# Performance work log

Measured on AMD Instinct MI355X. Metric: run time of the kernel, lower is better.

The kernel has to match this reference:

```python
import jax, jax.numpy as jnp
import numpy as np

ALPHA = 0.2  # LeakyReLU negative slope


def _gat_layer(x, edge_src, edge_dst, edge_embed, a, a2, concat):
    # torch: edge_h = cat(input[edge[0]], input[edge[1]], edge_embed).t(); scatter rows = edge[0]
    h = jnp.concatenate([x[edge_src], x[edge_dst], edge_embed], axis=1)  # [E, 2F+R]
    edge_m = h @ a.T                                                      # [E, D]
    powers = -jax.nn.leaky_relu(edge_m @ a2, ALPHA)                       # [E]
    edge_e = jnp.exp(powers)                                              # [E]
    N = x.shape[0]
    rowsum = jax.ops.segment_sum(edge_e, edge_src, num_segments=N)        # [N]
    rowsum = jnp.where(rowsum == 0.0, 1e-12, rowsum)
    h_prime = jax.ops.segment_sum(edge_e[:, None] * edge_m, edge_src, num_segments=N)  # [N, D]
    h_prime = h_prime / rowsum[:, None]
    return jax.nn.elu(h_prime) if concat else h_prime


def _spgat_forward(entity_embeddings, relation_embed, edge_embed, a, a2, W,
                   a_out, a2_out, edge_list, edge_type, edge_list_nhop, edge_type_nhop):
    nheads = a.shape[0]
    # concatenate 1-hop and n-hop edges (as in torch forward of the attention layer)
    src = jnp.concatenate([edge_list[0], edge_list_nhop[0]], axis=0)
    dst = jnp.concatenate([edge_list[1], edge_list_nhop[1]], axis=0)
    ee_nhop = relation_embed[edge_type_nhop[:, 0]] + relation_embed[edge_type_nhop[:, 1]]
    ee_all = jnp.concatenate([edge_embed, ee_nhop], axis=0)               # [E+E2, R]
    heads = [_gat_layer(entity_embeddings, src, dst, ee_all, a[i], a2[i], True)
             for i in range(nheads)]
    x = jnp.concatenate(heads, axis=1)                                    # [N, H*F] (dropout = identity, eval)
    out_relation_1 = relation_embed @ W                                   # [n_rel, H*F]
    ee2 = out_relation_1[edge_type]
    ee2_nhop = out_relation_1[edge_type_nhop[:, 0]] + out_relation_1[edge_type_nhop[:, 1]]
    ee2_all = jnp.concatenate([ee2, ee2_nhop], axis=0)                    # [E+E2, H*F]
    x = jax.nn.elu(_gat_layer(x, src, dst, ee2_all, a_out, a2_out, False))
    return x, out_relation_1


def setup_inputs() -> dict:
    key = jax.random.key(0)
    N, F, R, NREL, E, E2, H = 50000, 128, 128, 500, 150000, 30000, 2
    ks = jax.random.split(key, 12)

    def xavier(k, shape):
        fan_in, fan_out = shape[-1], shape[-2]
        std = 1.414 * np.sqrt(2.0 / (fan_in + fan_out))
        return (jax.random.normal(k, shape, dtype=jnp.float32) * std).astype(jnp.float32)

    return {
        "entity_embeddings": jax.random.normal(ks[0], (N, F), dtype=jnp.float32),
        "relation_embed": jax.random.normal(ks[1], (NREL, R), dtype=jnp.float32),
        "edge_embed": jax.random.normal(ks[2], (E, R), dtype=jnp.float32),
        "edge_list": jax.random.randint(ks[3], (2, E), 0, N),
        "edge_type": jax.random.randint(ks[4], (E,), 0, NREL),
        "edge_list_nhop": jax.random.randint(ks[5], (2, E2), 0, N),
        "edge_type_nhop": jax.random.randint(ks[6], (E2, 2), 0, NREL),
        "a": xavier(ks[7], (H, F, 2 * F + R)),            # per-head a: [D, 2F+R]
        "a2": xavier(ks[8], (H, 1, F))[:, 0, :],          # per-head a_2: [D]
        "W": xavier(ks[9], (R, H * F)),
        "a_out": xavier(ks[10], (H * F, 3 * H * F)),      # out layer: in=H*F, nrela=H*F
        "a2_out": xavier(ks[11], (1, H * F))[0],
    }


def reference(entity_embeddings, relation_embed, edge_embed, edge_list, edge_type,
              edge_list_nhop, edge_type_nhop, a, a2, W, a_out, a2_out):
    return _spgat_forward(entity_embeddings, relation_embed, edge_embed, a, a2, W,
                          a_out, a2_out, edge_list, edge_type, edge_list_nhop, edge_type_nhop)
```

## Files before the change

### kernel.cpp

```cpp
#include <hip/hip_runtime.h>
#include <cstdint>
#include <cstddef>

#define N_NODES 50000
#define MP1     50048
#define NRELC   500
#define E1      150000
#define MP2     150016
#define E2N     30000
#define ETOT    180000
#define ALPHA_F 0.2f
#define NBSCAN  49

typedef __attribute__((ext_vector_type(8))) short bf16x8;
typedef __attribute__((ext_vector_type(4))) float f32x4;

__device__ __forceinline__ float bf2f(unsigned short s) {
  return __uint_as_float((unsigned)s << 16);
}
__device__ __forceinline__ unsigned short f2bf(float f) {
  unsigned u = __float_as_uint(f);
  u += 0x7fff + ((u >> 16) & 1);
  return (unsigned short)(u >> 16);
}

__global__ void zero_int(int* __restrict__ p, int n) {
  int i = blockIdx.x * blockDim.x + threadIdx.x;
  if (i < n) p[i] = 0;
}

__global__ void build_count(const int* __restrict__ el, const int* __restrict__ elnh,
                            int* __restrict__ src, int* __restrict__ dst,
                            int* __restrict__ cnt) {
  int e = blockIdx.x * blockDim.x + threadIdx.x;
  if (e >= ETOT) return;
  int s, d;
  if (e < E1) { s = el[e];  d = el[E1 + e]; }
  else        { int k = e - E1; s = elnh[k]; d = elnh[E2N + k]; }
  src[e] = s; dst[e] = d;
  atomicAdd(&cnt[s], 1);
}

__global__ __launch_bounds__(256) void block_scan(const int* __restrict__ cnt,
                                                  int* __restrict__ rowptr,
                                                  int* __restrict__ blocksum) {
  __shared__ int wsum[4];
  const int tid  = threadIdx.x;
  const int lane = tid & 63;
  const int wave = tid >> 6;
  const int idx  = blockIdx.x * 1024 + tid * 4;
  int v0 = 0, v1 = 0, v2 = 0, v3 = 0;
  if (idx + 3 < N_NODES) {
    int4 t = *reinterpret_cast<const int4*>(cnt + idx);
    v0 = t.x; v1 = t.y; v2 = t.z; v3 = t.w;
  } else {
    if (idx + 0 < N_NODES) v0 = cnt[idx + 0];
    if (idx + 1 < N_NODES) v1 = cnt[idx + 1];
    if (idx + 2 < N_NODES) v2 = cnt[idx + 2];
  }
  const int tsum = v0 + v1 + v2 + v3;
  int incl = tsum;
#pragma unroll
  for (int off = 1; off < 64; off <<= 1) {
    int u = __shfl_up(incl, off);
    if (lane >= off) incl += u;
  }
  if (lane == 63) wsum[wave] = incl;
  __syncthreads();
  int woff = 0;
#pragma unroll
  for (int w = 0; w < 4; ++w)
    if (w < wave) woff += wsum[w];
  const int ebase = woff + incl - tsum;
  if (idx + 0 < N_NODES) rowptr[idx + 0] = ebase;
  if (idx + 1 < N_NODES) rowptr[idx + 1] = ebase + v0;
  if (idx + 2 < N_NODES) rowptr[idx + 2] = ebase + v0 + v1;
  if (idx + 3 < N_NODES) rowptr[idx + 3] = ebase + v0 + v1 + v2;
  if (tid == 255) blocksum[blockIdx.x] = woff + incl;
}

__global__ void scan_blocksums(int* __restrict__ blocksum, int* __restrict__ rowptr) {
  const int lane = threadIdx.x & 63;
  int v = (lane < NBSCAN) ? blocksum[lane] : 0;
  int incl = v;
#pragma unroll
  for (int off = 1; off < 64; off <<= 1) {
    int u = __shfl_up(incl, off);
    if (lane >= off) incl += u;
  }
  if (lane < NBSCAN) blocksum[lane] = incl - v;
  if (lane == 63) rowptr[N_NODES] = incl;
}

__global__ void add_offsets(int* __restrict__ rowptr, const int* __restrict__ blocksum,
                            int* __restrict__ pos) {
  int i = blockIdx.x * 256 + threadIdx.x;
  if (i < N_NODES) {
    int r = rowptr[i] + blocksum[i >> 10];
    rowptr[i] = r;
    pos[i] = r;
  }
}

__global__ void fill_csr(const int* __restrict__ src, int* __restrict__ pos, int* __restrict__ csr) {
  int e = blockIdx.x * blockDim.x + threadIdx.x;
  if (e >= ETOT) return;
  int p = atomicAdd(&pos[src[e]], 1);
  csr[p] = e;
}

#define PK_TOT (32768 + 32768 + 65536 + 65536 + 32768 + 131072)
__global__ void pack_all(const float* __restrict__ a, const float* __restrict__ W,
                         const float* __restrict__ ao,
                         float* __restrict__ weea3f, float* __restrict__ wtw,
                         float* __restrict__ wa3o,
                         unsigned short* __restrict__ wxa_bf,
                         unsigned short* __restrict__ weea3_bf,
                         unsigned short* __restrict__ wx1a_bf) {
  int i = blockIdx.x * blockDim.x + threadIdx.x;
  if (i >= PK_TOT) return;
  if (i < 32768) {
    int c = i >> 7, k = i & 127;
    int h = c >> 7, d = c & 127;
    weea3f[i] = a[h * 49152 + d * 384 + 256 + k];
  } else if (i < 65536) {
    int j = i - 32768;
    int n = j >> 7, k = j & 127;
    wtw[j] = W[k * 256 + n];
  } else if (i < 131072) {
    int j = i - 65536;
    int d = j >> 8, k = j & 255;
    wa3o[j] = ao[d * 768 + 512 + k];
  } else if (i < 196608) {
    int j = i - 131072;
    int c = j >> 7, k = j & 127;
    int h = c >> 8, part = (c >> 7) & 1, d = c & 127;
    wxa_bf[j] = f2bf(a[h * 49152 + d * 384 + part * 128 + k]);
  } else if (i < 229376) {
    int j = i - 196608;
    int c = j >> 7, k = j & 127;
    int h = c >> 7, d = c & 127;
    weea3_bf[j] = f2bf(a[h * 49152 + d * 384 + 256 + k]);
  } else {
    int j = i - 229376;
    int c = j >> 8, k = j & 255;
    int part = c >> 8, d = c & 255;
    wx1a_bf[j] = f2bf(ao[d * 768 + part * 256 + k]);
  }
}

__global__ __launch_bounds__(256) void gemm_bt_f32(
    const float* __restrict__ A, const float* __restrict__ Wt,
    float* __restrict__ C, int M, int N, int K) {
  __shared__ float As[32][132];
  __shared__ float Bs[32][132];
  const int bm = blockIdx.x * 128;
  const int bn = blockIdx.y * 128;
  const int tid = threadIdx.x;
  const int tx = tid & 15;
  const int ty = tid >> 4;
  float acc[8][8];
#pragma unroll
  for (int i = 0; i < 8; ++i)
#pragma unroll
    for (int j = 0; j < 8; ++j) acc[i][j] = 0.f;

  const int lr = tid >> 3;
  const int lc = (tid & 7) << 2;

  for (int k0 = 0; k0 < K; k0 += 32) {
#pragma unroll
    for (int i = 0; i < 4; ++i) {
      const int row = lr + (i << 5);
      float4 av = make_float4(0.f, 0.f, 0.f, 0.f);
      float4 bv = make_float4(0.f, 0.f, 0.f, 0.f);
      const int ga = bm + row, gb = bn + row;
      if (ga < M) av = *reinterpret_cast<const float4*>(A + (size_t)ga * K + k0 + lc);
      if (gb < N) bv = *reinterpret_cast<const float4*>(Wt + (size_t)gb * K + k0 + lc);
      As[lc + 0][row] = av.x; As[lc + 1][row] = av.y; As[lc + 2][row] = av.z; As[lc + 3][row] = av.w;
      Bs[lc + 0][row] = bv.x; Bs[lc + 1][row] = bv.y; Bs[lc + 2][row] = bv.z; Bs[lc + 3][row] = bv.w;
    }
    __syncthreads();
    for (int kk = 0; kk < 32; ++kk) {
      float a8[8], b8[8];
      *(float4*)&a8[0] = *(const float4*)&As[kk][ty * 8];
      *(float4*)&a8[4] = *(const float4*)&As[kk][ty * 8 + 4];
      *(float4*)&b8[0] = *(const float4*)&Bs[kk][tx * 8];
      *(float4*)&b8[4] = *(const float4*)&Bs[kk][tx * 8 + 4];
#pragma unroll
      for (int i = 0; i < 8; ++i)
#pragma unroll
        for (int j = 0; j < 8; ++j) acc[i][j] = fmaf(a8[i], b8[j], acc[i][j]);
    }
    __syncthreads();
  }
#pragma unroll
  for (int i = 0; i < 8; ++i) {
    const int gr = bm + ty * 8 + i;
    if (gr < M) {
      float4 v0 = make_float4(acc[i][0], acc[i][1], acc[i][2], acc[i][3]);
      float4 v1 = make_float4(acc[i][4], acc[i][5], acc[i][6], acc[i][7]);
      *reinterpret_cast<float4*>(C + (size_t)gr * N + bn + tx * 8) = v0;
      *reinterpret_cast<float4*>(C + (size_t)gr * N + bn + tx * 8 + 4) = v1;
    }
  }
}

template <typename TA, int K>
__global__ __launch_bounds__(256) void gemm_mfma(
    const TA* __restrict__ A, const unsigned short* __restrict__ Wt,
    unsigned short* __restrict__ C, int Mreal, int N) {
  __shared__ __align__(16) unsigned short lds[2][8192];
  const int tid  = threadIdx.x;
  const int wave = tid >> 6;
  const int lane = tid & 63;
  const int bm = blockIdx.x * 128;
  const int bn = blockIdx.y * 128;
  const int wr = wave >> 1, wc = wave & 1;
  constexpr int NT = K / 32;

  f32x4 acc[4][4] = {};

  const int rb   = lane & 15;
  const int cofs = ((lane >> 4) ^ (lane & 3)) << 3;

  auto stageB = [&](int buf, int kt) {
#pragma unroll
    for (int j = 0; j < 2; ++j) {
      const int o   = (wave * 2 + j) * 1024 + lane * 16;
      const int row = o >> 6;
      const int sc  = (o & 63) ^ ((row & 3) << 4);
      const char* g = (const char*)Wt + (size_t)(bn + row) * (K * 2) + kt * 64 + sc;
      __builtin_amdgcn_global_load_lds(
          (const __attribute__((address_space(1))) void*)g,
          (__attribute__((address_space(3))) void*)&lds[buf][4096 + (wave * 2 + j) * 512],
          16, 0, 0);
    }
  };
  auto stageA = [&](int buf, int kt) {
    if constexpr (sizeof(TA) == 2) {
#pragma unroll
      for (int j = 0; j < 2; ++j) {
        const int o   = (wave * 2 + j) * 1024 + lane * 16;
        const int row = o >> 6;
        const int sc  = (o & 63) ^ ((row & 3) << 4);
        const char* g = (const char*)A + (size_t)(bm + row) * (K * 2) + kt * 64 + sc;
        __builtin_amdgcn_global_load_lds(
            (const __attribute__((address_space(1))) void*)g,
            (__attribute__((address_space(3))) void*)&lds[buf][(wave * 2 + j) * 512],
            16, 0, 0);
      }
    } else {
#pragma unroll
      for (int p = 0; p < 2; ++p) {
        const int o   = p * 4096 + tid * 16;
        const int row = o >> 6;
        const int ke  = ((o & 63) ^ ((row & 3) << 4)) >> 1;
        const int gr  = bm + row;
        float v[8];
#pragma unroll
        for (int q = 0; q < 8; ++q) v[q] = 0.f;
        if (gr < Mreal) {
          const float* gp = (const float*)A + (size_t)gr * K + kt * 32 + ke;
          float4 u0 = *(const float4*)gp;
          float4 u1 = *(const float4*)(gp + 4);
          v[0] = u0.x; v[1] = u0.y; v[2] = u0.z; v[3] = u0.w;
          v[4] = u1.x; v[5] = u1.y; v[6] = u1.z; v[7] = u1.w;
        }
        bf16x8 pk;
#pragma unroll
        for (int q = 0; q < 8; ++q) pk[q] = (short)f2bf(v[q]);
        *(bf16x8*)&lds[buf][o >> 1] = pk;
      }
    }
  };

  stageA(0, 0); stageB(0, 0);
  for (int t = 0; t < NT; ++t) {
    __syncthreads();
    if (t + 1 < NT) { stageA((t + 1) & 1, t + 1); stageB((t + 1) & 1, t + 1); }
    const int buf = t & 1;
    bf16x8 af[4], bfr[4];
#pragma unroll
    for (int m = 0; m < 4; ++m)
      af[m] = *(const bf16x8*)&lds[buf][(rb + 16 * m + 64 * wr) * 32 + cofs];
#pragma unroll
    for (int n = 0; n < 4; ++n)
      bfr[n] = *(const bf16x8*)&lds[buf][4096 + (rb + 16 * n + 64 * wc) * 32 + cofs];
#pragma unroll
    for (int m = 0; m < 4; ++m)
#pragma unroll
      for (int n = 0; n < 4; ++n)
        acc[m][n] = __builtin_amdgcn_mfma_f32_16x16x32_bf16(af[m], bfr[n], acc[m][n], 0, 0, 0);
  }

  const int ccol = bn + wc * 64 + rb;
  const int crow = bm + wr * 64 + ((lane >> 4) << 2);
#pragma unroll
  for (int m = 0; m < 4; ++m)
#pragma unroll
    for (int n = 0; n < 4; ++n)
#pragma unroll
      for (int r = 0; r < 4; ++r)
        C[(size_t)(crow + 16 * m + r) * N + ccol + 16 * n] = f2bf(acc[m][n][r]);
}

__global__ __launch_bounds__(256) void agg1(
    const unsigned short* __restrict__ xa, const unsigned short* __restrict__ eeA31,
    const float* __restrict__ relA3, const int* __restrict__ rowptr,
    const int* __restrict__ csr, const int* __restrict__ dst,
    const int* __restrict__ etnh, const float* __restrict__ a2,
    unsigned short* __restrict__ x1) {
  int w = blockIdx.x * 4 + (threadIdx.x >> 6);
  int n = w >> 1, h = w & 1;
  if (n >= N_NODES) return;
  int l = threadIdx.x & 63;
  float w2a = a2[h * 128 + l];
  float w2b = a2[h * 128 + 64 + l];
  const unsigned short* xan = xa + (size_t)n * 512 + h * 256;
  float s0 = bf2f(xan[l]), s1 = bf2f(xan[64 + l]);
  float acc0 = 0.f, acc1 = 0.f, rs = 0.f;
  int p0 = rowptr[n], p1 = rowptr[n + 1];
  for (int p = p0; p < p1; ++p) {
    int e = csr[p];
    int d = dst[e];
    const unsigned short* xad = xa + (size_t)d * 512 + h * 256 + 128;
    float m0 = s0 + bf2f(xad[l]);
    float m1 = s1 + bf2f(xad[64 + l]);
    if (e < E1) {
      const unsigned short* ee = eeA31 + (size_t)e * 256 + h * 128;
      m0 += bf2f(ee[l]); m1 += bf2f(ee[64 + l]);
    } else {
      int k = e - E1;
      int t0 = etnh[2 * k], t1 = etnh[2 * k + 1];
      const float* r0 = relA3 + t0 * 256 + h * 128;
      const float* r1 = relA3 + t1 * 256 + h * 128;
      m0 += r0[l] + r1[l];
      m1 += r0[64 + l] + r1[64 + l];
    }
    float dot = m0 * w2a + m1 * w2b;
#pragma unroll
    for (int off = 32; off; off >>= 1) dot += __shfl_xor(dot, off);
    float lk = dot > 0.f ? dot : ALPHA_F * dot;
    float ev = __expf(-lk);
    acc0 = fmaf(ev, m0, acc0);
    acc1 = fmaf(ev, m1, acc1);
    rs += ev;
  }
  if (rs == 0.f) rs = 1e-12f;
  float inv = 1.f / rs;
  float h0 = acc0 * inv, h1 = acc1 * inv;
  h0 = h0 > 0.f ? h0 : (__expf(h0) - 1.f);
  h1 = h1 > 0.f ? h1 : (__expf(h1) - 1.f);
  x1[(size_t)n * 256 + h * 128 + l] = f2bf(h0);
  x1[(size_t)n * 256 + h * 128 + 64 + l] = f2bf(h1);
}

__global__ __launch_bounds__(256) void agg2(
    const unsigned short* __restrict__ x1a, const float* __restrict__ rel2,
    const int* __restrict__ rowptr, const int* __restrict__ csr,
    const int* __restrict__ dst, const int* __restrict__ etype,
    const int* __restrict__ etnh, const float* __restrict__ a2o,
    float* __restrict__ out) {
  int n = blockIdx.x * 4 + (threadIdx.x >> 6);
  if (n >= N_NODES) return;
  int l = threadIdx.x & 63;
  float w2[4], s[4], acc[4] = {0.f, 0.f, 0.f, 0.f};
#pragma unroll
  for (int j = 0; j < 4; ++j) {
    w2[j] = a2o[j * 64 + l];
    s[j] = bf2f(x1a[(size_t)n * 512 + j * 64 + l]);
  }
  float rs = 0.f;
  int p0 = rowptr[n], p1 = rowptr[n + 1];
  for (int p = p0; p < p1; ++p) {
    int e = csr[p];
    int d = dst[e];
    const unsigned short* xd = x1a + (size_t)d * 512 + 256;
    float m[4];
    if (e < E1) {
      int t = etype[e];
      const float* r = rel2 + t * 256;
#pragma unroll
      for (int j = 0; j < 4; ++j) m[j] = s[j] + bf2f(xd[j * 64 + l]) + r[j * 64 + l];
    } else {
      int k = e - E1;
      int t0 = etnh[2 * k], t1 = etnh[2 * k + 1];
      const float* r0 = rel2 + t0 * 256;
      const float* r1 = rel2 + t1 * 256;
#pragma unroll
      for (int j = 0; j < 4; ++j) m[j] = s[j] + bf2f(xd[j * 64 + l]) + r0[j * 64 + l] + r1[j * 64 + l];
    }
    float dot = 0.f;
#pragma unroll
    for (int j = 0; j < 4; ++j) dot = fmaf(m[j], w2[j], dot);
#pragma unroll
    for (int off = 32; off; off >>= 1) dot += __shfl_xor(dot, off);
    float lk = dot > 0.f ? dot : ALPHA_F * dot;
    float ev = __expf(-lk);
#pragma unroll
    for (int j = 0; j < 4; ++j) acc[j] = fmaf(ev, m[j], acc[j]);
    rs += ev;
  }
  if (rs == 0.f) rs = 1e-12f;
  float inv = 1.f / rs;
#pragma unroll
  for (int j = 0; j < 4; ++j) {
    float hv = acc[j] * inv;
    hv = hv > 0.f ? hv : (__expf(hv) - 1.f);
    out[(size_t)n * 256 + j * 64 + l] = hv;
  }
}

extern "C" void kernel_launch(void* const* d_in, const int* in_sizes, int n_in,
                              void* d_out, int out_size, void* d_ws, size_t ws_size,
                              hipStream_t stream) {
  const float* x    = (const float*)d_in[0];
  const float* rel  = (const float*)d_in[1];
  const float* eemb = (const float*)d_in[2];
  const int*   el   = (const int*)d_in[3];
  const int*   et   = (const int*)d_in[4];
  const int*   elnh = (const int*)d_in[5];
  const int*   etnh = (const int*)d_in[6];
  const float* a    = (const float*)d_in[7];
  const float* a2   = (const float*)d_in[8];
  const float* W    = (const float*)d_in[9];
  const float* aout = (const float*)d_in[10];
  const float* a2o  = (const float*)d_in[11];

  char* ws = (char*)d_ws;
  size_t cur = 0;
  auto alloc = [&](size_t bytes) {
    size_t o = cur;
    cur = (cur + bytes + 511) & ~(size_t)511;
    return o;
  };
  int* src     = (int*)(ws + alloc((size_t)ETOT * 4));
  int* dstv    = (int*)(ws + alloc((size_t)ETOT * 4));
  int* rowptr  = (int*)(ws + alloc((size_t)(N_NODES + 1) * 4));
  int* pos     = (int*)(ws + alloc((size_t)N_NODES * 4));
  int* csr     = (int*)(ws + alloc((size_t)ETOT * 4));
  int* bsum    = (int*)(ws + alloc((size_t)64 * 4));
  float* weea3f = (float*)(ws + alloc((size_t)256 * 128 * 4));
  float* wtw    = (float*)(ws + alloc((size_t)256 * 128 * 4));
  float* wa3o   = (float*)(ws + alloc((size_t)256 * 256 * 4));
  unsigned short* wxa_bf   = (unsigned short*)(ws + alloc((size_t)512 * 128 * 2));
  unsigned short* weea3_bf = (unsigned short*)(ws + alloc((size_t)256 * 128 * 2));
  unsigned short* wx1a_bf  = (unsigned short*)(ws + alloc((size_t)512 * 256 * 2));
  float* relA3 = (float*)(ws + alloc((size_t)NRELC * 256 * 4));
  float* rel2  = (float*)(ws + alloc((size_t)NRELC * 256 * 4));
  unsigned short* x1B = (unsigned short*)(ws + alloc((size_t)MP1 * 256 * 2));
  unsigned short* xaB = (unsigned short*)(ws + alloc((size_t)MP1 * 512 * 2));
  unsigned short* eeB = (unsigned short*)(ws + alloc((size_t)MP2 * 256 * 2));
  (void)ws_size; (void)in_sizes; (void)n_in; (void)out_size;

  float* out_x    = (float*)d_out;
  float* out_rel1 = out_x + (size_t)N_NODES * 256;

  zero_int<<<(N_NODES + 255) / 256, 256, 0, stream>>>(pos, N_NODES);
  build_count<<<(ETOT + 255) / 256, 256, 0, stream>>>(el, elnh, src, dstv, pos);
  block_scan<<<NBSCAN, 256, 0, stream>>>(pos, rowptr, bsum);
  scan_blocksums<<<1, 64, 0, stream>>>(bsum, rowptr);
  add_offsets<<<(N_NODES + 255) / 256, 256, 0, stream>>>(rowptr, bsum, pos);
  fill_csr<<<(ETOT + 255) / 256, 256, 0, stream>>>(src, pos, csr);

  pack_all<<<(PK_TOT + 255) / 256, 256, 0, stream>>>(a, W, aout, weea3f, wtw, wa3o,
                                                     wxa_bf, weea3_bf, wx1a_bf);

  gemm_mfma<float, 128><<<dim3(MP1 / 128, 4), 256, 0, stream>>>(x, wxa_bf, xaB, N_NODES, 512);
  gemm_mfma<float, 128><<<dim3(MP2 / 128, 2), 256, 0, stream>>>(eemb, weea3_bf, eeB, E1, 256);
  gemm_bt_f32<<<dim3((NRELC + 127) / 128, 2), 256, 0, stream>>>(rel, weea3f, relA3, NRELC, 256, 128);

  agg1<<<(N_NODES * 2 + 3) / 4, 256, 0, stream>>>(xaB, eeB, relA3, rowptr, csr, dstv, etnh, a2, x1B);

  gemm_bt_f32<<<dim3((NRELC + 127) / 128, 2), 256, 0, stream>>>(rel, wtw, out_rel1, NRELC, 256, 128);
  gemm_bt_f32<<<dim3((NRELC + 127) / 128, 2), 256, 0, stream>>>(out_rel1, wa3o, rel2, NRELC, 256, 256);

  gemm_mfma<unsigned short, 256><<<dim3(MP1 / 128, 4), 256, 0, stream>>>(x1B, wx1a_bf, xaB, MP1, 512);

  agg2<<<(N_NODES + 3) / 4, 256, 0, stream>>>(xaB, rel2, rowptr, csr, dstv, et, etnh, a2o, out_x);
}
```

Measured before the change: 496.4 us.

## Precompute attention logits via folded a2·A vectors and batch edge gathers

```diff
diff --git a/kernel.cpp b/kernel.cpp
--- a/kernel.cpp
+++ b/kernel.cpp
@@ -11,6 +11,7 @@
 #define ETOT    180000
 #define ALPHA_F 0.2f
 #define NBSCAN  49
+#define NDBLK   ((N_NODES + 3) / 4)
 
 typedef __attribute__((ext_vector_type(8))) short bf16x8;
 typedef __attribute__((ext_vector_type(4))) float f32x4;
@@ -109,14 +110,18 @@
   csr[p] = e;
 }
 
-#define PK_TOT (32768 + 32768 + 65536 + 65536 + 32768 + 131072)
+#define PK_COPY (32768 + 32768 + 65536 + 65536 + 32768 + 131072)
+#define PK_TOT  (PK_COPY + 768 + 768)
 __global__ void pack_all(const float* __restrict__ a, const float* __restrict__ W,
-                         const float* __restrict__ ao,
+                         const float* __restrict__ ao, const float* __restrict__ a2,
+                         const float* __restrict__ a2o,
                          float* __restrict__ weea3f, float* __restrict__ wtw,
                          float* __restrict__ wa3o,
                          unsigned short* __restrict__ wxa_bf,
                          unsigned short* __restrict__ weea3_bf,
-                         unsigned short* __restrict__ wx1a_bf) {
+                         unsigned short* __restrict__ wx1a_bf,
+                         float* __restrict__ vaL1,
+                         float* __restrict__ vaL2) {
   int i = blockIdx.x * blockDim.x + threadIdx.x;
   if (i >= PK_TOT) return;
   if (i < 32768) {
@@ -141,11 +146,25 @@
     int c = j >> 7, k = j & 127;
     int h = c >> 7, d = c & 127;
     weea3_bf[j] = f2bf(a[h * 49152 + d * 384 + 256 + k]);
-  } else {
+  } else if (i < PK_COPY) {
     int j = i - 229376;
     int c = j >> 8, k = j & 255;
     int part = c >> 8, d = c & 255;
     wx1a_bf[j] = f2bf(ao[d * 768 + part * 256 + k]);
+  } else if (i < PK_COPY + 768) {
+    int j = i - PK_COPY;
+    int v = j >> 8, rem = j & 255, h = rem >> 7, k = rem & 127;
+    float s = 0.f;
+    for (int d = 0; d < 128; ++d)
+      s = fmaf(a2[h * 128 + d], a[h * 49152 + d * 384 + v * 128 + k], s);
+    vaL1[(v * 2 + h) * 128 + k] = s;
+  } else {
+    int j = i - PK_COPY - 768;
+    int v = j >> 8, k = j & 255;
+    float s = 0.f;
+    for (int d = 0; d < 256; ++d)
+      s = fmaf(a2o[d], ao[d * 768 + v * 256 + k], s);
+    vaL2[v * 256 + k] = s;
   }
 }
 
@@ -206,10 +225,12 @@
   }
 }
 
-template <typename TA, int K>
+template <typename TA, int K, int NS>
 __global__ __launch_bounds__(256) void gemm_mfma(
     const TA* __restrict__ A, const unsigned short* __restrict__ Wt,
-    unsigned short* __restrict__ C, int Mreal, int N) {
+    unsigned short* __restrict__ C,
+    const float* __restrict__ va, float* __restrict__ sout,
+    int Mreal, int N) {
   __shared__ __align__(16) unsigned short lds[2][8192];
   const int tid  = threadIdx.x;
   const int wave = tid >> 6;
@@ -220,6 +241,14 @@
   constexpr int NT = K / 32;
 
   f32x4 acc[4][4] = {};
+  float sacc[2][NS > 0 ? NS : 1];
+  if constexpr (NS > 0) {
+#pragma unroll
+    for (int p = 0; p < 2; ++p)
+#pragma unroll
+      for (int s = 0; s < NS; ++s) sacc[p][s] = 0.f;
+  }
+  const bool do_s = (NS > 0) && (blockIdx.y == 0);
 
   const int rb   = lane & 15;
   const int cofs = ((lane >> 4) ^ (lane & 3)) << 3;
@@ -267,6 +296,15 @@
           v[0] = u0.x; v[1] = u0.y; v[2] = u0.z; v[3] = u0.w;
           v[4] = u1.x; v[5] = u1.y; v[6] = u1.z; v[7] = u1.w;
         }
+        if constexpr (NS > 0) {
+          if (do_s) {
+#pragma unroll
+            for (int s = 0; s < NS; ++s)
+#pragma unroll
+              for (int q = 0; q < 8; ++q)
+                sacc[p][s] = fmaf(v[q], va[s * K + kt * 32 + ke + q], sacc[p][s]);
+          }
+        }
         bf16x8 pk;
 #pragma unroll
         for (int q = 0; q < 8; ++q) pk[q] = (short)f2bf(v[q]);
@@ -294,6 +332,22 @@
         acc[m][n] = __builtin_amdgcn_mfma_f32_16x16x32_bf16(af[m], bfr[n], acc[m][n], 0, 0, 0);
   }
 
+  if constexpr (NS > 0) {
+    if (do_s) {
+#pragma unroll
+      for (int p = 0; p < 2; ++p) {
+        const int row = bm + p * 64 + (tid >> 2);
+#pragma unroll
+        for (int s = 0; s < NS; ++s) {
+          float vv = sacc[p][s];
+          vv += __shfl_xor(vv, 1);
+          vv += __shfl_xor(vv, 2);
+          if ((tid & 3) == 0 && row < Mreal) sout[(size_t)row * NS + s] = vv;
+        }
+      }
+    }
+  }
+
   const int ccol = bn + wc * 64 + rb;
   const int crow = bm + wr * 64 + ((lane >> 4) << 2);
 #pragma unroll
@@ -305,51 +359,139 @@
         C[(size_t)(crow + 16 * m + r) * N + ccol + 16 * n] = f2bf(acc[m][n][r]);
 }
 
+__global__ void rel_dots1(const float* __restrict__ rel, const float* __restrict__ vaL1,
+                          float* __restrict__ srel1) {
+  int r = blockIdx.x * 4 + (threadIdx.x >> 6);
+  if (r >= NRELC) return;
+  int l = threadIdx.x & 63;
+  float r0 = rel[r * 128 + l], r1 = rel[r * 128 + 64 + l];
+  const float* vee0 = vaL1 + 4 * 128;
+  const float* vee1 = vaL1 + 5 * 128;
+  float p0 = r0 * vee0[l] + r1 * vee0[64 + l];
+  float p1 = r0 * vee1[l] + r1 * vee1[64 + l];
+#pragma unroll
+  for (int off = 32; off; off >>= 1) { p0 += __shfl_xor(p0, off); p1 += __shfl_xor(p1, off); }
+  if (l == 0) { srel1[r * 2 + 0] = p0; srel1[r * 2 + 1] = p1; }
+}
+
+__global__ void edge_logits1(const int* __restrict__ src, const int* __restrict__ dst,
+                             const int* __restrict__ etnh,
+                             const float* __restrict__ s12, const float* __restrict__ s3,
+                             const float* __restrict__ srel1, float* __restrict__ ew) {
+  int e = blockIdx.x * 256 + threadIdx.x;
+  if (e >= ETOT) return;
+  int s = src[e], d = dst[e];
+  float e0, e1;
+  if (e < E1) { e0 = s3[e * 2 + 0]; e1 = s3[e * 2 + 1]; }
+  else {
+    int k = e - E1;
+    int t0 = etnh[2 * k], t1 = etnh[2 * k + 1];
+    e0 = srel1[t0 * 2 + 0] + srel1[t1 * 2 + 0];
+    e1 = srel1[t0 * 2 + 1] + srel1[t1 * 2 + 1];
+  }
+  float l0 = s12[(size_t)s * 4 + 0] + s12[(size_t)d * 4 + 2] + e0;
+  float l1 = s12[(size_t)s * 4 + 1] + s12[(size_t)d * 4 + 3] + e1;
+  l0 = l0 > 0.f ? l0 : ALPHA_F * l0;
+  l1 = l1 > 0.f ? l1 : ALPHA_F * l1;
+  ew[(size_t)e * 2 + 0] = __expf(-l0);
+  ew[(size_t)e * 2 + 1] = __expf(-l1);
+}
+
+__global__ void post_dots(const unsigned short* __restrict__ x1, const float* __restrict__ vaL2,
+                          const float* __restrict__ or1,
+                          float* __restrict__ t12, float* __restrict__ trel2) {
+  int b = blockIdx.x;
+  int wv = threadIdx.x >> 6, l = threadIdx.x & 63;
+  if (b < NDBLK) {
+    int n = b * 4 + wv;
+    if (n >= N_NODES) return;
+    const unsigned short* row = x1 + (size_t)n * 256;
+    ushort4 u = *reinterpret_cast<const ushort4*>(row + l * 4);
+    float p1 = 0.f, p2 = 0.f;
+    const float* va1o = vaL2;
+    const float* va2o = vaL2 + 256;
+    float xv0 = bf2f(u.x), xv1 = bf2f(u.y), xv2 = bf2f(u.z), xv3 = bf2f(u.w);
+    p1 = xv0 * va1o[l * 4] + xv1 * va1o[l * 4 + 1] + xv2 * va1o[l * 4 + 2] + xv3 * va1o[l * 4 + 3];
+    p2 = xv0 * va2o[l * 4] + xv1 * va2o[l * 4 + 1] + xv2 * va2o[l * 4 + 2] + xv3 * va2o[l * 4 + 3];
+#pragma unroll
+    for (int off = 32; off; off >>= 1) { p1 += __shfl_xor(p1, off); p2 += __shfl_xor(p2, off); }
+    if (l == 0) { t12[(size_t)n * 2 + 0] = p1; t12[(size_t)n * 2 + 1] = p2; }
+  } else {
+    int r = (b - NDBLK) * 4 + wv;
+    if (r >= NRELC) return;
+    const float* row = or1 + (size_t)r * 256;
+    float4 f = *reinterpret_cast<const float4*>(row + l * 4);
+    const float* va3o = vaL2 + 512;
+    float p = f.x * va3o[l * 4] + f.y * va3o[l * 4 + 1] + f.z * va3o[l * 4 + 2] + f.w * va3o[l * 4 + 3];
+#pragma unroll
+    for (int off = 32; off; off >>= 1) p += __shfl_xor(p, off);
+    if (l == 0) trel2[r] = p;
+  }
+}
+
+__global__ void edge_logits2(const int* __restrict__ src, const int* __restrict__ dst,
+                             const int* __restrict__ etype, const int* __restrict__ etnh,
+                             const float* __restrict__ t12, const float* __restrict__ trel2,
+                             float* __restrict__ ew2) {
+  int e = blockIdx.x * 256 + threadIdx.x;
+  if (e >= ETOT) return;
+  int s = src[e], d = dst[e];
+  float tr;
+  if (e < E1) tr = trel2[etype[e]];
+  else {
+    int k = e - E1;
+    tr = trel2[etnh[2 * k]] + trel2[etnh[2 * k + 1]];
+  }
+  float lg = t12[(size_t)s * 2 + 0] + t12[(size_t)d * 2 + 1] + tr;
+  lg = lg > 0.f ? lg : ALPHA_F * lg;
+  ew2[e] = __expf(-lg);
+}
+
 __global__ __launch_bounds__(256) void agg1(
-    const unsigned short* __restrict__ xa, const unsigned short* __restrict__ eeA31,
-    const float* __restrict__ relA3, const int* __restrict__ rowptr,
-    const int* __restrict__ csr, const int* __restrict__ dst,
-    const int* __restrict__ etnh, const float* __restrict__ a2,
+    const unsigned short* __restrict__ xa, const unsigned short* __restrict__ eeB,
+    const float* __restrict__ relA3, const float* __restrict__ ew,
+    const int* __restrict__ rowptr, const int* __restrict__ csr,
+    const int* __restrict__ dstv, const int* __restrict__ etnh,
     unsigned short* __restrict__ x1) {
-  int w = blockIdx.x * 4 + (threadIdx.x >> 6);
-  int n = w >> 1, h = w & 1;
+  int w_ = blockIdx.x * 4 + (threadIdx.x >> 6);
+  int n = w_ >> 1, h = w_ & 1;
   if (n >= N_NODES) return;
   int l = threadIdx.x & 63;
-  float w2a = a2[h * 128 + l];
-  float w2b = a2[h * 128 + 64 + l];
   const unsigned short* xan = xa + (size_t)n * 512 + h * 256;
   float s0 = bf2f(xan[l]), s1 = bf2f(xan[64 + l]);
   float acc0 = 0.f, acc1 = 0.f, rs = 0.f;
   int p0 = rowptr[n], p1 = rowptr[n + 1];
-  for (int p = p0; p < p1; ++p) {
-    int e = csr[p];
-    int d = dst[e];
-    const unsigned short* xad = xa + (size_t)d * 512 + h * 256 + 128;
-    float m0 = s0 + bf2f(xad[l]);
-    float m1 = s1 + bf2f(xad[64 + l]);
-    if (e < E1) {
-      const unsigned short* ee = eeA31 + (size_t)e * 256 + h * 128;
-      m0 += bf2f(ee[l]); m1 += bf2f(ee[64 + l]);
-    } else {
-      int k = e - E1;
-      int t0 = etnh[2 * k], t1 = etnh[2 * k + 1];
-      const float* r0 = relA3 + t0 * 256 + h * 128;
-      const float* r1 = relA3 + t1 * 256 + h * 128;
-      m0 += r0[l] + r1[l];
-      m1 += r0[64 + l] + r1[64 + l];
-    }
-    float dot = m0 * w2a + m1 * w2b;
-#pragma unroll
-    for (int off = 32; off; off >>= 1) dot += __shfl_xor(dot, off);
-    float lk = dot > 0.f ? dot : ALPHA_F * dot;
-    float ev = __expf(-lk);
-    acc0 = fmaf(ev, m0, acc0);
-    acc1 = fmaf(ev, m1, acc1);
-    rs += ev;
-  }
-  if (rs == 0.f) rs = 1e-12f;
-  float inv = 1.f / rs;
-  float h0 = acc0 * inv, h1 = acc1 * inv;
+  for (int p = p0; p < p1; p += 4) {
+    int e[4], d[4]; float wv[4];
+#pragma unroll
+    for (int j = 0; j < 4; ++j) { int pp = p + j; e[j] = csr[pp < p1 ? pp : p0]; }
+#pragma unroll
+    for (int j = 0; j < 4; ++j) d[j] = dstv[e[j]];
+#pragma unroll
+    for (int j = 0; j < 4; ++j) wv[j] = (p + j < p1) ? ew[(size_t)e[j] * 2 + h] : 0.f;
+#pragma unroll
+    for (int j = 0; j < 4; ++j) {
+      const unsigned short* xad = xa + (size_t)d[j] * 512 + h * 256 + 128;
+      float m0 = bf2f(xad[l]), m1 = bf2f(xad[64 + l]);
+      if (e[j] < E1) {
+        const unsigned short* ee = eeB + (size_t)e[j] * 256 + h * 128;
+        m0 += bf2f(ee[l]); m1 += bf2f(ee[64 + l]);
+      } else {
+        int k = e[j] - E1;
+        const float* r0 = relA3 + etnh[2 * k] * 256 + h * 128;
+        const float* r1 = relA3 + etnh[2 * k + 1] * 256 + h * 128;
+        m0 += r0[l] + r1[l];
+        m1 += r0[64 + l] + r1[64 + l];
+      }
+      acc0 = fmaf(wv[j], m0, acc0);
+      acc1 = fmaf(wv[j], m1, acc1);
+      rs += wv[j];
+    }
+  }
+  bool deg = p1 > p0;
+  float inv = deg ? 1.f / rs : 0.f;
+  float h0 = deg ? (s0 + acc0 * inv) : 0.f;
+  float h1 = deg ? (s1 + acc1 * inv) : 0.f;
   h0 = h0 > 0.f ? h0 : (__expf(h0) - 1.f);
   h1 = h1 > 0.f ? h1 : (__expf(h1) - 1.f);
   x1[(size_t)n * 256 + h * 128 + l] = f2bf(h0);
@@ -358,57 +500,53 @@
 
 __global__ __launch_bounds__(256) void agg2(
     const unsigned short* __restrict__ x1a, const float* __restrict__ rel2,
+    const float* __restrict__ ew2,
     const int* __restrict__ rowptr, const int* __restrict__ csr,
-    const int* __restrict__ dst, const int* __restrict__ etype,
-    const int* __restrict__ etnh, const float* __restrict__ a2o,
-    float* __restrict__ out) {
+    const int* __restrict__ dstv, const int* __restrict__ etype,
+    const int* __restrict__ etnh, float* __restrict__ out) {
   int n = blockIdx.x * 4 + (threadIdx.x >> 6);
   if (n >= N_NODES) return;
   int l = threadIdx.x & 63;
-  float w2[4], s[4], acc[4] = {0.f, 0.f, 0.f, 0.f};
-#pragma unroll
-  for (int j = 0; j < 4; ++j) {
-    w2[j] = a2o[j * 64 + l];
-    s[j] = bf2f(x1a[(size_t)n * 512 + j * 64 + l]);
-  }
+  float s[4], acc[4] = {0.f, 0.f, 0.f, 0.f};
+#pragma unroll
+  for (int j = 0; j < 4; ++j) s[j] = bf2f(x1a[(size_t)n * 512 + j * 64 + l]);
   float rs = 0.f;
   int p0 = rowptr[n], p1 = rowptr[n + 1];
-  for (int p = p0; p < p1; ++p) {
-    int e = csr[p];
-    int d = dst[e];
-    const unsigned short* xd = x1a + (size_t)d * 512 + 256;
-    float m[4];
-    if (e < E1) {
-      int t = etype[e];
-      const float* r = rel2 + t * 256;
-#pragma unroll
-      for (int j = 0; j < 4; ++j) m[j] = s[j] + bf2f(xd[j * 64 + l]) + r[j * 64 + l];
-    } else {
-      int k = e - E1;
-      int t0 = etnh[2 * k], t1 = etnh[2 * k + 1];
-      const float* r0 = rel2 + t0 * 256;
-      const float* r1 = rel2 + t1 * 256;
-#pragma unroll
-      for (int j = 0; j < 4; ++j) m[j] = s[j] + bf2f(xd[j * 64 + l]) + r0[j * 64 + l] + r1[j * 64 + l];
-    }
-    float dot = 0.f;
-#pragma unroll
-    for (int j = 0; j < 4; ++j) dot = fmaf(m[j], w2[j], dot);
-#pragma unroll
-    for (int off = 32; off; off >>= 1) dot += __shfl_xor(dot, off);
-    float lk = dot > 0.f ? dot : ALPHA_F * dot;
-    float ev = __expf(-lk);
-#pragma unroll
-    for (int j = 0; j < 4; ++j) acc[j] = fmaf(ev, m[j], acc[j]);
-    rs += ev;
-  }
-  if (rs == 0.f) rs = 1e-12f;
-  float inv = 1.f / rs;
-#pragma unroll
-  for (int j = 0; j < 4; ++j) {
-    float hv = acc[j] * inv;
+  for (int p = p0; p < p1; p += 4) {
+    int e[4], d[4]; float wv[4];
+#pragma unroll
+    for (int j = 0; j < 4; ++j) { int pp = p + j; e[j] = csr[pp < p1 ? pp : p0]; }
+#pragma unroll
+    for (int j = 0; j < 4; ++j) d[j] = dstv[e[j]];
+#pragma unroll
+    for (int j = 0; j < 4; ++j) wv[j] = (p + j < p1) ? ew2[e[j]] : 0.f;
+#pragma unroll
+    for (int j = 0; j < 4; ++j) {
+      const unsigned short* xd = x1a + (size_t)d[j] * 512 + 256;
+      float m[4];
+      if (e[j] < E1) {
+        const float* r = rel2 + (size_t)etype[e[j]] * 256;
+#pragma unroll
+        for (int q = 0; q < 4; ++q) m[q] = bf2f(xd[q * 64 + l]) + r[q * 64 + l];
+      } else {
+        int k = e[j] - E1;
+        const float* r0 = rel2 + (size_t)etnh[2 * k] * 256;
+        const float* r1 = rel2 + (size_t)etnh[2 * k + 1] * 256;
+#pragma unroll
+        for (int q = 0; q < 4; ++q) m[q] = bf2f(xd[q * 64 + l]) + r0[q * 64 + l] + r1[q * 64 + l];
+      }
+#pragma unroll
+      for (int q = 0; q < 4; ++q) acc[q] = fmaf(wv[j], m[q], acc[q]);
+      rs += wv[j];
+    }
+  }
+  bool deg = p1 > p0;
+  float inv = deg ? 1.f / rs : 0.f;
+#pragma unroll
+  for (int q = 0; q < 4; ++q) {
+    float hv = deg ? (s[q] + acc[q] * inv) : 0.f;
     hv = hv > 0.f ? hv : (__expf(hv) - 1.f);
-    out[(size_t)n * 256 + j * 64 + l] = hv;
+    out[(size_t)n * 256 + q * 64 + l] = hv;
   }
 }
 
@@ -449,6 +587,15 @@
   unsigned short* wx1a_bf  = (unsigned short*)(ws + alloc((size_t)512 * 256 * 2));
   float* relA3 = (float*)(ws + alloc((size_t)NRELC * 256 * 4));
   float* rel2  = (float*)(ws + alloc((size_t)NRELC * 256 * 4));
+  float* vaL1  = (float*)(ws + alloc((size_t)6 * 128 * 4));
+  float* vaL2  = (float*)(ws + alloc((size_t)3 * 256 * 4));
+  float* s12   = (float*)(ws + alloc((size_t)MP1 * 4 * 4));
+  float* s3    = (float*)(ws + alloc((size_t)E1 * 2 * 4));
+  float* srel1 = (float*)(ws + alloc((size_t)NRELC * 2 * 4));
+  float* trel2 = (float*)(ws + alloc((size_t)NRELC * 4));
+  float* t12   = (float*)(ws + alloc((size_t)N_NODES * 2 * 4));
+  float* ew    = (float*)(ws + alloc((size_t)ETOT * 2 * 4));
+  float* ew2   = (float*)(ws + alloc((size_t)ETOT * 4));
   unsigned short* x1B = (unsigned short*)(ws + alloc((size_t)MP1 * 256 * 2));
   unsigned short* xaB = (unsigned short*)(ws + alloc((size_t)MP1 * 512 * 2));
   unsigned short* eeB = (unsigned short*)(ws + alloc((size_t)MP2 * 256 * 2));
@@ -464,19 +611,25 @@
   add_offsets<<<(N_NODES + 255) / 256, 256, 0, stream>>>(rowptr, bsum, pos);
   fill_csr<<<(ETOT + 255) / 256, 256, 0, stream>>>(src, pos, csr);
 
-  pack_all<<<(PK_TOT + 255) / 256, 256, 0, stream>>>(a, W, aout, weea3f, wtw, wa3o,
-                                                     wxa_bf, weea3_bf, wx1a_bf);
-
-  gemm_mfma<float, 128><<<dim3(MP1 / 128, 4), 256, 0, stream>>>(x, wxa_bf, xaB, N_NODES, 512);
-  gemm_mfma<float, 128><<<dim3(MP2 / 128, 2), 256, 0, stream>>>(eemb, weea3_bf, eeB, E1, 256);
+  pack_all<<<(PK_TOT + 255) / 256, 256, 0, stream>>>(a, W, aout, a2, a2o,
+                                                     weea3f, wtw, wa3o,
+                                                     wxa_bf, weea3_bf, wx1a_bf, vaL1, vaL2);
+
+  gemm_mfma<float, 128, 4><<<dim3(MP1 / 128, 4), 256, 0, stream>>>(x, wxa_bf, xaB, vaL1, s12, N_NODES, 512);
+  gemm_mfma<float, 128, 2><<<dim3(MP2 / 128, 2), 256, 0, stream>>>(eemb, weea3_bf, eeB, vaL1 + 4 * 128, s3, E1, 256);
   gemm_bt_f32<<<dim3((NRELC + 127) / 128, 2), 256, 0, stream>>>(rel, weea3f, relA3, NRELC, 256, 128);
-
-  agg1<<<(N_NODES * 2 + 3) / 4, 256, 0, stream>>>(xaB, eeB, relA3, rowptr, csr, dstv, etnh, a2, x1B);
 
   gemm_bt_f32<<<dim3((NRELC + 127) / 128, 2), 256, 0, stream>>>(rel, wtw, out_rel1, NRELC, 256, 128);
   gemm_bt_f32<<<dim3((NRELC + 127) / 128, 2), 256, 0, stream>>>(out_rel1, wa3o, rel2, NRELC, 256, 256);
 
-  gemm_mfma<unsigned short, 256><<<dim3(MP1 / 128, 4), 256, 0, stream>>>(x1B, wx1a_bf, xaB, MP1, 512);
-
-  agg2<<<(N_NODES + 3) / 4, 256, 0, stream>>>(xaB, rel2, rowptr, csr, dstv, et, etnh, a2o, out_x);
-}
+  rel_dots1<<<(NRELC + 3) / 4, 256, 0, stream>>>(rel, vaL1, srel1);
+  edge_logits1<<<(ETOT + 255) / 256, 256, 0, stream>>>(src, dstv, etnh, s12, s3, srel1, ew);
+  agg1<<<(N_NODES * 2 + 3) / 4, 256, 0, stream>>>(xaB, eeB, relA3, ew, rowptr, csr, dstv, etnh, x1B);
+
+  post_dots<<<NDBLK + (NRELC + 3) / 4, 256, 0, stream>>>(x1B, vaL2, out_rel1, t12, trel2);
+  edge_logits2<<<(ETOT + 255) / 256, 256, 0, stream>>>(src, dstv, et, etnh, t12, trel2, ew2);
+
+  gemm_mfma<unsigned short, 256, 0><<<dim3(MP1 / 128, 4), 256, 0, stream>>>(x1B, wx1a_bf, xaB, nullptr, nullptr, MP1, 512);
+
+  agg2<<<(N_NODES + 3) / 4, 256, 0, stream>>>(xaB, rel2, ew2, rowptr, csr, dstv, et, etnh, out_x);
+}
```

Result: slower. 518.1 us (+4.4%).
